# Kernel tuning notes

Measured on AMD Instinct MI355X. Metric: run time of the kernel, lower is better.

Reference implementation:

```python
import jax, jax.numpy as jnp
import numpy as np

B, D, H, G, E = 32768, 256, 256, 8, 8  # batch, input_size, hidden_size, num_groups, experts_per_group


def setup_inputs() -> dict:
    key = jax.random.key(0)
    ks = jax.random.split(key, 5)
    s_d = 1.0 / np.sqrt(D)
    return {
        "x": jax.random.normal(ks[0], (B, D), dtype=jnp.float32),
        # gate: nn.Linear(D, G*E)
        "W_gate": jax.random.uniform(ks[1], (G * E, D), jnp.float32, -s_d, s_d),
        "b_gate": jax.random.uniform(ks[2], (G * E,), jnp.float32, -s_d, s_d),
        # experts: [G, E] x nn.Linear(D, H)
        "W_exp": jax.random.uniform(ks[3], (G, E, H, D), jnp.float32, -s_d, s_d),
        "b_exp": jax.random.uniform(ks[4], (G, E, H), jnp.float32, -s_d, s_d),
    }


def reference(x, W_gate, b_gate, W_exp, b_exp):
    # gate_outputs = softmax(gate(x), dim=1)  -> [B, G*E]
    gate = jax.nn.softmax(x @ W_gate.T + b_gate, axis=1)
    # per-group sum over experts of Linear(x): contract input dim i and expert dim e
    # [B, G, H]
    group_out = jnp.einsum("bi,gehi->bgh", x, W_exp) + b_exp.sum(axis=1)
    expert_flat = group_out.reshape(x.shape[0], -1)  # [B, G*H]
    # output = sum_g gate[b,g] * expert_flat[b,h]  == gate.sum(1) * expert_flat
    # (avoids materializing the [B, G*E, G*H] broadcast the torch code creates)
    out = gate.sum(axis=1, keepdims=True) * expert_flat
    return out
```

## Files before the change

kernel.cpp:

```cpp
#include <hip/hip_runtime.h>


typedef unsigned short u16;
typedef __bf16 bf16x8 __attribute__((ext_vector_type(8)));
typedef float f32x4 __attribute__((ext_vector_type(4)));

#define MB 32768
#define NN 2048
#define KK 256
#define BK 64

__device__ __forceinline__ u16 f2bf(float f) {
    unsigned u = __builtin_bit_cast(unsigned, f);
    u += 0x7FFFu + ((u >> 16) & 1u);
    return (u16)(u >> 16);
}

__device__ __forceinline__ void gld16(const void* g, void* l) {
    __builtin_amdgcn_global_load_lds((const __attribute__((address_space(1))) void*)g,
                                     (__attribute__((address_space(3))) void*)l,
                                     16, 0, 0);
}

__global__ __launch_bounds__(256) void prep_kernel(
    const float* __restrict__ x, const float* __restrict__ Wexp,
    const float* __restrict__ bexp, u16* __restrict__ xb,
    u16* __restrict__ Ws, float* __restrict__ bs)
{
    const int blk = blockIdx.x;
    const int t = threadIdx.x;
    if (blk < 512) {
        const int tid = blk * 256 + t;
        const int n = tid >> 6;
        const int i = (tid & 63) << 2;
        const int g = n >> 8, h = n & 255;
        const float* base = Wexp + ((size_t)(g * 8) * 256 + h) * 256 + i;
        float s0 = 0.f, s1 = 0.f, s2 = 0.f, s3 = 0.f;
#pragma unroll
        for (int e = 0; e < 8; ++e) {
            const float4 v = *(const float4*)(base + (size_t)e * 65536);
            s0 += v.x; s1 += v.y; s2 += v.z; s3 += v.w;
        }
        ushort4 o;
        o.x = f2bf(s0); o.y = f2bf(s1); o.z = f2bf(s2); o.w = f2bf(s3);
        *(ushort4*)(Ws + (size_t)n * KK + i) = o;
        if ((tid & 63) == 0) {
            float sb = 0.f;
#pragma unroll
            for (int e = 0; e < 8; ++e) sb += bexp[(g * 8 + e) * 256 + h];
            bs[n] = sb;
        }
    } else {
        int idx = (blk - 512) * 256 + t;
        const float4* xv = (const float4*)x;
#pragma unroll
        for (int it = 0; it < 4; ++it) {
            const int j = idx + it * 524288;
            const float4 v = xv[j];
            ushort4 o;
            o.x = f2bf(v.x); o.y = f2bf(v.y); o.z = f2bf(v.z); o.w = f2bf(v.w);
            *(ushort4*)(xb + (size_t)j * 4) = o;
        }
    }
}

__global__ __launch_bounds__(256, 3) void gemm_kernel(
    const u16* __restrict__ A, const u16* __restrict__ Bt,
    const float* __restrict__ bias, float* __restrict__ C)
{
    __shared__ __align__(16) u16 sA[128 * BK];
    __shared__ __align__(16) u16 sB[128 * BK];

    const int t = threadIdx.x;
    const int n0 = blockIdx.x * 128;
    const int m0 = blockIdx.y * 128;

    const int lane = t & 63;
    const int w = t >> 6;
    const int wm = (w & 1) << 6;
    const int wn = (w >> 1) << 6;
    const int lr = lane & 15;
    const int quad = lane >> 4;

    f32x4 acc[4][4] = {};

    const int srow = t >> 3;
    const int scs  = t & 7;

    for (int k0 = 0; k0 < KK; k0 += BK) {
#pragma unroll
        for (int r = 0; r < 4; ++r) {
            const int row = srow + r * 32;
            const int gc  = ((scs ^ (row & 7)) << 3);
            gld16(A  + (size_t)(m0 + row) * KK + k0 + gc, sA + (size_t)(r * 256 + t) * 8);
            gld16(Bt + (size_t)(n0 + row) * KK + k0 + gc, sB + (size_t)(r * 256 + t) * 8);
        }
        __syncthreads();

#pragma unroll
        for (int kk = 0; kk < 2; ++kk) {
            bf16x8 af[4], bf[4];
#pragma unroll
            for (int mi = 0; mi < 4; ++mi) {
                const int rr = wm + mi * 16 + lr;
                const int c  = (kk * 4 + quad) ^ (rr & 7);
                af[mi] = *(const bf16x8*)(sA + rr * BK + (c << 3));
            }
#pragma unroll
            for (int ni = 0; ni < 4; ++ni) {
                const int rr = wn + ni * 16 + lr;
                const int c  = (kk * 4 + quad) ^ (rr & 7);
                bf[ni] = *(const bf16x8*)(sB + rr * BK + (c << 3));
            }
#pragma unroll
            for (int mi = 0; mi < 4; ++mi)
#pragma unroll
                for (int ni = 0; ni < 4; ++ni)
                    acc[mi][ni] = __builtin_amdgcn_mfma_f32_16x16x32_bf16(
                        af[mi], bf[ni], acc[mi][ni], 0, 0, 0);
        }
        __syncthreads();
    }

#pragma unroll
    for (int ni = 0; ni < 4; ++ni) {
        const int col = n0 + wn + ni * 16 + lr;
        const float bv = bias[col];
#pragma unroll
        for (int mi = 0; mi < 4; ++mi) {
            const int row = m0 + wm + mi * 16 + quad * 4;
            float* Cp = C + (size_t)row * NN + col;
#pragma unroll
            for (int r = 0; r < 4; ++r)
                Cp[(size_t)r * NN] = acc[mi][ni][r] + bv;
        }
    }
}

extern "C" void kernel_launch(void* const* d_in, const int* in_sizes, int n_in,
                              void* d_out, int out_size, void* d_ws, size_t ws_size,
                              hipStream_t stream) {
    const float* x    = (const float*)d_in[0];
    const float* Wexp = (const float*)d_in[3];
    const float* bexp = (const float*)d_in[4];
    float* out = (float*)d_out;

    u16*   xb = (u16*)d_ws;
    u16*   Ws = (u16*)((char*)d_ws + (size_t)16777216);
    float* bs = (float*)((char*)d_ws + (size_t)16777216 + 1048576);

    prep_kernel<<<2560, 256, 0, stream>>>(x, Wexp, bexp, xb, Ws, bs);
    dim3 grid(NN / 128, MB / 128);
    gemm_kernel<<<grid, 256, 0, stream>>>(xb, Ws, bs, out);
}
```

Before: 334.4 us.

## Fuse x fp32-to-bf16 conversion into GEMM A-tile load and remap blocks per XCD

Removes the separate pass that converted x to bf16 in workspace. The GEMM now loads fp32 x directly, packs it to bf16 with v_cvt_pk_bf16_f32, and stores it into swizzled LDS. The grid is flattened, and block indices are remapped so that each XCD processes a contiguous range of tiles, improving L2 reuse of x rows. In exchange, A-tile loads go through registers synchronously instead of async global-to-LDS loads, and each x tile is read in fp32 by several n-blocks.

```diff
diff --git a/kernel.cpp b/kernel.cpp
--- a/kernel.cpp
+++ b/kernel.cpp
@@ -16,6 +16,12 @@
     return (u16)(u >> 16);
 }
 
+__device__ __forceinline__ unsigned cvtpk(float lo, float hi) {
+    unsigned r;
+    asm("v_cvt_pk_bf16_f32 %0, %1, %2" : "=v"(r) : "v"(lo), "v"(hi));
+    return r;
+}
+
 __device__ __forceinline__ void gld16(const void* g, void* l) {
     __builtin_amdgcn_global_load_lds((const __attribute__((address_space(1))) void*)g,
                                      (__attribute__((address_space(3))) void*)l,
@@ -23,57 +29,44 @@
 }
 
 __global__ __launch_bounds__(256) void prep_kernel(
-    const float* __restrict__ x, const float* __restrict__ Wexp,
-    const float* __restrict__ bexp, u16* __restrict__ xb,
+    const float* __restrict__ Wexp, const float* __restrict__ bexp,
     u16* __restrict__ Ws, float* __restrict__ bs)
 {
-    const int blk = blockIdx.x;
-    const int t = threadIdx.x;
-    if (blk < 512) {
-        const int tid = blk * 256 + t;
-        const int n = tid >> 6;
-        const int i = (tid & 63) << 2;
-        const int g = n >> 8, h = n & 255;
-        const float* base = Wexp + ((size_t)(g * 8) * 256 + h) * 256 + i;
-        float s0 = 0.f, s1 = 0.f, s2 = 0.f, s3 = 0.f;
+    const int tid = blockIdx.x * 256 + threadIdx.x;
+    const int n = tid >> 6;
+    const int i = (tid & 63) << 2;
+    const int g = n >> 8, h = n & 255;
+    const float* base = Wexp + ((size_t)(g * 8) * 256 + h) * 256 + i;
+    float s0 = 0.f, s1 = 0.f, s2 = 0.f, s3 = 0.f;
 #pragma unroll
-        for (int e = 0; e < 8; ++e) {
-            const float4 v = *(const float4*)(base + (size_t)e * 65536);
-            s0 += v.x; s1 += v.y; s2 += v.z; s3 += v.w;
-        }
-        ushort4 o;
-        o.x = f2bf(s0); o.y = f2bf(s1); o.z = f2bf(s2); o.w = f2bf(s3);
-        *(ushort4*)(Ws + (size_t)n * KK + i) = o;
-        if ((tid & 63) == 0) {
-            float sb = 0.f;
+    for (int e = 0; e < 8; ++e) {
+        const float4 v = *(const float4*)(base + (size_t)e * 65536);
+        s0 += v.x; s1 += v.y; s2 += v.z; s3 += v.w;
+    }
+    ushort4 o;
+    o.x = f2bf(s0); o.y = f2bf(s1); o.z = f2bf(s2); o.w = f2bf(s3);
+    *(ushort4*)(Ws + (size_t)n * KK + i) = o;
+    if ((tid & 63) == 0) {
+        float sb = 0.f;
 #pragma unroll
-            for (int e = 0; e < 8; ++e) sb += bexp[(g * 8 + e) * 256 + h];
-            bs[n] = sb;
-        }
-    } else {
-        int idx = (blk - 512) * 256 + t;
-        const float4* xv = (const float4*)x;
-#pragma unroll
-        for (int it = 0; it < 4; ++it) {
-            const int j = idx + it * 524288;
-            const float4 v = xv[j];
-            ushort4 o;
-            o.x = f2bf(v.x); o.y = f2bf(v.y); o.z = f2bf(v.z); o.w = f2bf(v.w);
-            *(ushort4*)(xb + (size_t)j * 4) = o;
-        }
+        for (int e = 0; e < 8; ++e) sb += bexp[(g * 8 + e) * 256 + h];
+        bs[n] = sb;
     }
 }
 
 __global__ __launch_bounds__(256, 3) void gemm_kernel(
-    const u16* __restrict__ A, const u16* __restrict__ Bt,
+    const float* __restrict__ X, const u16* __restrict__ Bt,
     const float* __restrict__ bias, float* __restrict__ C)
 {
     __shared__ __align__(16) u16 sA[128 * BK];
     __shared__ __align__(16) u16 sB[128 * BK];
 
     const int t = threadIdx.x;
-    const int n0 = blockIdx.x * 128;
-    const int m0 = blockIdx.y * 128;
+
+    const int bid  = blockIdx.x;
+    const int rmap = (bid & 7) * 512 + (bid >> 3);
+    const int n0 = (rmap & 15) << 7;
+    const int m0 = (rmap >> 4) << 7;
 
     const int lane = t & 63;
     const int w = t >> 6;
@@ -92,8 +85,25 @@
         for (int r = 0; r < 4; ++r) {
             const int row = srow + r * 32;
             const int gc  = ((scs ^ (row & 7)) << 3);
-            gld16(A  + (size_t)(m0 + row) * KK + k0 + gc, sA + (size_t)(r * 256 + t) * 8);
             gld16(Bt + (size_t)(n0 + row) * KK + k0 + gc, sB + (size_t)(r * 256 + t) * 8);
+        }
+        f32x4 va[8];
+#pragma unroll
+        for (int r = 0; r < 4; ++r) {
+            const float* src = X + (size_t)(m0 + srow + r * 32) * KK + k0 + (scs << 3);
+            va[2 * r]     = *(const f32x4*)(src);
+            va[2 * r + 1] = *(const f32x4*)(src + 4);
+        }
+#pragma unroll
+        for (int r = 0; r < 4; ++r) {
+            const int row = srow + r * 32;
+            const int sc  = (scs ^ (row & 7)) << 3;
+            uint4 pk;
+            pk.x = cvtpk(va[2 * r][0], va[2 * r][1]);
+            pk.y = cvtpk(va[2 * r][2], va[2 * r][3]);
+            pk.z = cvtpk(va[2 * r + 1][0], va[2 * r + 1][1]);
+            pk.w = cvtpk(va[2 * r + 1][2], va[2 * r + 1][3]);
+            *(uint4*)(sA + row * BK + sc) = pk;
         }
         __syncthreads();
 
@@ -145,11 +155,10 @@
     const float* bexp = (const float*)d_in[4];
     float* out = (float*)d_out;
 
-    u16*   xb = (u16*)d_ws;
-    u16*   Ws = (u16*)((char*)d_ws + (size_t)16777216);
-    float* bs = (float*)((char*)d_ws + (size_t)16777216 + 1048576);
+    u16*   Ws = (u16*)d_ws;
+    float* bs = (float*)((char*)d_ws + 1048576);
 
-    prep_kernel<<<2560, 256, 0, stream>>>(x, Wexp, bexp, xb, Ws, bs);
-    dim3 grid(NN / 128, MB / 128);
-    gemm_kernel<<<grid, 256, 0, stream>>>(xb, Ws, bs, out);
+    prep_kernel<<<512, 256, 0, stream>>>(Wexp, bexp, Ws, bs);
+    dim3 grid(4096);
+    gemm_kernel<<<grid, 256, 0, stream>>>(x, Ws, bs, out);
 }
```

Measured after the change: 378.3 us. 13.1% more time.

## Double-buffer LDS tiles and vectorize output stores via swapped MFMA operands

Applied to the files above, without the earlier changes.

Double-buffers the shared-memory A/B tiles so the next K-slice's global-to-LDS loads overlap the current slice's MFMAs. Waits use explicit vmcnt counts and raw barriers instead of __syncthreads. It also swaps the MFMA operand order so each lane holds four consecutive columns, which allows 16-byte float4 stores of the output and the bias. LDS use doubles and launch bounds drop to two blocks per CU, lowering occupancy in exchange for the overlap and wider writes.

```diff
diff --git a/kernel.cpp b/kernel.cpp
--- a/kernel.cpp
+++ b/kernel.cpp
@@ -64,12 +64,12 @@
     }
 }
 
-__global__ __launch_bounds__(256, 3) void gemm_kernel(
+__global__ __launch_bounds__(256, 2) void gemm_kernel(
     const u16* __restrict__ A, const u16* __restrict__ Bt,
     const float* __restrict__ bias, float* __restrict__ C)
 {
-    __shared__ __align__(16) u16 sA[128 * BK];
-    __shared__ __align__(16) u16 sB[128 * BK];
+    __shared__ __align__(16) u16 sA[2][128 * BK];
+    __shared__ __align__(16) u16 sB[2][128 * BK];
 
     const int t = threadIdx.x;
     const int n0 = blockIdx.x * 128;
@@ -87,15 +87,30 @@
     const int srow = t >> 3;
     const int scs  = t & 7;
 
-    for (int k0 = 0; k0 < KK; k0 += BK) {
+#define STAGE(P, K0)                                                              \
+    {                                                                             \
+        _Pragma("unroll")                                                         \
+        for (int r = 0; r < 4; ++r) {                                             \
+            const int row = srow + r * 32;                                        \
+            const int gc  = ((scs ^ (row & 7)) << 3);                             \
+            gld16(A  + (size_t)(m0 + row) * KK + (K0) + gc,                       \
+                  sA[P] + (size_t)(r * 256 + t) * 8);                             \
+            gld16(Bt + (size_t)(n0 + row) * KK + (K0) + gc,                       \
+                  sB[P] + (size_t)(r * 256 + t) * 8);                             \
+        }                                                                         \
+    }
+
+    STAGE(0, 0);
+    int p = 0;
 #pragma unroll
-        for (int r = 0; r < 4; ++r) {
-            const int row = srow + r * 32;
-            const int gc  = ((scs ^ (row & 7)) << 3);
-            gld16(A  + (size_t)(m0 + row) * KK + k0 + gc, sA + (size_t)(r * 256 + t) * 8);
-            gld16(Bt + (size_t)(n0 + row) * KK + k0 + gc, sB + (size_t)(r * 256 + t) * 8);
+    for (int it = 0; it < 4; ++it) {
+        if (it < 3) {
+            STAGE(p ^ 1, (it + 1) * BK);
+            asm volatile("s_waitcnt vmcnt(8)" ::: "memory");
+        } else {
+            asm volatile("s_waitcnt vmcnt(0)" ::: "memory");
         }
-        __syncthreads();
+        __builtin_amdgcn_s_barrier();
 
 #pragma unroll
         for (int kk = 0; kk < 2; ++kk) {
@@ -104,35 +119,36 @@
             for (int mi = 0; mi < 4; ++mi) {
                 const int rr = wm + mi * 16 + lr;
                 const int c  = (kk * 4 + quad) ^ (rr & 7);
-                af[mi] = *(const bf16x8*)(sA + rr * BK + (c << 3));
+                af[mi] = *(const bf16x8*)(sA[p] + rr * BK + (c << 3));
             }
 #pragma unroll
             for (int ni = 0; ni < 4; ++ni) {
                 const int rr = wn + ni * 16 + lr;
                 const int c  = (kk * 4 + quad) ^ (rr & 7);
-                bf[ni] = *(const bf16x8*)(sB + rr * BK + (c << 3));
+                bf[ni] = *(const bf16x8*)(sB[p] + rr * BK + (c << 3));
             }
 #pragma unroll
             for (int mi = 0; mi < 4; ++mi)
 #pragma unroll
                 for (int ni = 0; ni < 4; ++ni)
                     acc[mi][ni] = __builtin_amdgcn_mfma_f32_16x16x32_bf16(
-                        af[mi], bf[ni], acc[mi][ni], 0, 0, 0);
+                        bf[ni], af[mi], acc[mi][ni], 0, 0, 0);
         }
-        __syncthreads();
+        if (it < 3) __builtin_amdgcn_s_barrier();
+        p ^= 1;
     }
+#undef STAGE
 
 #pragma unroll
-    for (int ni = 0; ni < 4; ++ni) {
-        const int col = n0 + wn + ni * 16 + lr;
-        const float bv = bias[col];
+    for (int mi = 0; mi < 4; ++mi) {
+        const int row = m0 + wm + mi * 16 + lr;
+        float* Cp = C + (size_t)row * NN;
 #pragma unroll
-        for (int mi = 0; mi < 4; ++mi) {
-            const int row = m0 + wm + mi * 16 + quad * 4;
-            float* Cp = C + (size_t)row * NN + col;
-#pragma unroll
-            for (int r = 0; r < 4; ++r)
-                Cp[(size_t)r * NN] = acc[mi][ni][r] + bv;
+        for (int ni = 0; ni < 4; ++ni) {
+            const int col = n0 + wn + ni * 16 + quad * 4;
+            const f32x4 bv = *(const f32x4*)(bias + col);
+            f32x4 v = acc[mi][ni] + bv;
+            *(f32x4*)(Cp + col) = v;
         }
     }
 }
```

New measurement: 341.3 us. +2.1%, slower.

## Double-buffer A in LDS, load B directly to registers, vectorize stores

Applied to the files above, without the earlier changes.

The GEMM kernel now double-buffers the A tile in shared memory and prefetches the next K-step with an explicit vmcnt wait, so global loads overlap the MFMA work. B fragments are read straight from global memory into registers instead of going through LDS. The MFMA operands are swapped so the output is transposed, which lets each lane write a contiguous float4 plus a vector bias. The risks are higher register pressure under launch_bounds(256,3) and uncoalesced direct global reads of B.

```diff
diff --git a/kernel.cpp b/kernel.cpp
--- a/kernel.cpp
+++ b/kernel.cpp
@@ -68,8 +68,7 @@
     const u16* __restrict__ A, const u16* __restrict__ Bt,
     const float* __restrict__ bias, float* __restrict__ C)
 {
-    __shared__ __align__(16) u16 sA[128 * BK];
-    __shared__ __align__(16) u16 sB[128 * BK];
+    __shared__ __align__(16) u16 sA[2][128 * BK];
 
     const int t = threadIdx.x;
     const int n0 = blockIdx.x * 128;
@@ -87,52 +86,83 @@
     const int srow = t >> 3;
     const int scs  = t & 7;
 
-    for (int k0 = 0; k0 < KK; k0 += BK) {
-#pragma unroll
-        for (int r = 0; r < 4; ++r) {
-            const int row = srow + r * 32;
-            const int gc  = ((scs ^ (row & 7)) << 3);
-            gld16(A  + (size_t)(m0 + row) * KK + k0 + gc, sA + (size_t)(r * 256 + t) * 8);
-            gld16(Bt + (size_t)(n0 + row) * KK + k0 + gc, sB + (size_t)(r * 256 + t) * 8);
-        }
-        __syncthreads();
+    const u16* bbase = Bt + (size_t)(n0 + wn + lr) * KK + quad * 8;
+
+#define STAGEA(P, K0)                                                   \
+    {                                                                   \
+        _Pragma("unroll")                                               \
+        for (int r = 0; r < 4; ++r) {                                   \
+            const int row = srow + r * 32;                              \
+            const int gc  = ((scs ^ (row & 7)) << 3);                   \
+            gld16(A + (size_t)(m0 + row) * KK + (K0) + gc,              \
+                  sA[P] + (size_t)(r * 256 + t) * 8);                   \
+        }                                                               \
+    }
+
+#define LOADB(DST, K0)                                                  \
+    {                                                                   \
+        _Pragma("unroll")                                               \
+        for (int kk = 0; kk < 2; ++kk)                                  \
+            _Pragma("unroll")                                           \
+            for (int ni = 0; ni < 4; ++ni)                              \
+                DST[kk * 4 + ni] = *(const bf16x8*)(                    \
+                    bbase + (size_t)ni * 16 * KK + (K0) + kk * 32);     \
+    }
+
+    bf16x8 b0[8], b1[8];
+
+    STAGEA(0, 0);
+    LOADB(b0, 0);
+
+#define BODY(IT, P, BC, BN)                                             \
+    {                                                                   \
+        if ((IT) < 3) {                                                 \
+            STAGEA(P ^ 1, ((IT) + 1) * BK);                             \
+            LOADB(BN, ((IT) + 1) * BK);                                 \
+            asm volatile("s_waitcnt vmcnt(12)" ::: "memory");           \
+        } else {                                                        \
+            asm volatile("s_waitcnt vmcnt(0)" ::: "memory");            \
+        }                                                               \
+        __builtin_amdgcn_s_barrier();                                   \
+        _Pragma("unroll")                                               \
+        for (int kk = 0; kk < 2; ++kk) {                                \
+            bf16x8 af[4];                                               \
+            _Pragma("unroll")                                           \
+            for (int mi = 0; mi < 4; ++mi) {                            \
+                const int rr = wm + mi * 16 + lr;                       \
+                const int c  = (kk * 4 + quad) ^ (rr & 7);              \
+                af[mi] = *(const bf16x8*)(sA[P] + rr * BK + (c << 3));  \
+            }                                                           \
+             \
+            _Pragma("unroll")                                           \
+            for (int mi = 0; mi < 4; ++mi)                              \
+                _Pragma("unroll")                                       \
+                for (int ni = 0; ni < 4; ++ni)                          \
+                    acc[mi][ni] = __builtin_amdgcn_mfma_f32_16x16x32_bf16( \
+                        BC[kk * 4 + ni], af[mi], acc[mi][ni], 0, 0, 0); \
+        }                                                               \
+        if ((IT) < 3) __builtin_amdgcn_s_barrier();                     \
+    }
+
+    BODY(0, 0, b0, b1);
+    BODY(1, 1, b1, b0);
+    BODY(2, 0, b0, b1);
+    BODY(3, 1, b1, b0);
+
+#undef BODY
+#undef LOADB
+#undef STAGEA
 
 #pragma unroll
-        for (int kk = 0; kk < 2; ++kk) {
-            bf16x8 af[4], bf[4];
+    for (int mi = 0; mi < 4; ++mi) {
+        const int row = m0 + wm + mi * 16 + lr;
+        float* Cp = C + (size_t)row * NN;
 #pragma unroll
-            for (int mi = 0; mi < 4; ++mi) {
-                const int rr = wm + mi * 16 + lr;
-                const int c  = (kk * 4 + quad) ^ (rr & 7);
-                af[mi] = *(const bf16x8*)(sA + rr * BK + (c << 3));
-            }
-#pragma unroll
-            for (int ni = 0; ni < 4; ++ni) {
-                const int rr = wn + ni * 16 + lr;
-                const int c  = (kk * 4 + quad) ^ (rr & 7);
-                bf[ni] = *(const bf16x8*)(sB + rr * BK + (c << 3));
-            }
-#pragma unroll
-            for (int mi = 0; mi < 4; ++mi)
-#pragma unroll
-                for (int ni = 0; ni < 4; ++ni)
-                    acc[mi][ni] = __builtin_amdgcn_mfma_f32_16x16x32_bf16(
-                        af[mi], bf[ni], acc[mi][ni], 0, 0, 0);
-        }
-        __syncthreads();
-    }
-
-#pragma unroll
-    for (int ni = 0; ni < 4; ++ni) {
-        const int col = n0 + wn + ni * 16 + lr;
-        const float bv = bias[col];
-#pragma unroll
-        for (int mi = 0; mi < 4; ++mi) {
-            const int row = m0 + wm + mi * 16 + quad * 4;
-            float* Cp = C + (size_t)row * NN + col;
-#pragma unroll
-            for (int r = 0; r < 4; ++r)
-                Cp[(size_t)r * NN] = acc[mi][ni][r] + bv;
+        for (int ni = 0; ni < 4; ++ni) {
+            const int col = n0 + wn + ni * 16 + quad * 4;
+            const f32x4 bv = *(const f32x4*)(bias + col);
+            f32x4 v = acc[mi][ni] + bv;
+            *(f32x4*)(Cp + col) = v;
         }
     }
 }
```

New measurement: 368.2 us. +10.1%, slower.
